# Performance work log

Measured on AMD Instinct MI355X. Metric: run time of the kernel, lower is better.

## Reference

```python
import jax, jax.numpy as jnp
import numpy as np

TEMPERATURE = 8.0  # sqrt(d_head=64)
CLAMP = 15.0
EPS = 1e-6


def setup_inputs() -> dict:
    key = jax.random.key(0)
    kq, kk, kv, km = jax.random.split(key, 4)
    B, Lq, Lk, D = 16, 2048, 2048, 64
    q = jax.random.normal(kq, (B, Lq, D), dtype=jnp.float32)
    k = jax.random.normal(kk, (B, Lk, D), dtype=jnp.float32)
    v = jax.random.normal(kv, (B, Lk, D), dtype=jnp.float32)
    mask = jax.random.randint(km, (B, Lq, Lk), 0, 2).astype(jnp.float32)
    return {"q": q, "k": k, "v": v, "mask": mask}


def masked_softmax(x, m, axis=-1):
    # clamp -> multiply by mask -> stable exp -> multiply by mask -> normalize
    x = jnp.clip(x, -CLAMP, CLAMP)
    x = x * m
    e_x = jnp.exp(x - jnp.max(x, axis=axis, keepdims=True))
    e_x = e_x * m
    return e_x / (jnp.sum(e_x, axis=axis, keepdims=True) + EPS)


def reference(q, k, v, mask):
    # scores: [B, Lq, Lk]
    attn = jnp.einsum('bqd,bkd->bqk', q, k) / TEMPERATURE
    attn = masked_softmax(attn, mask, axis=2)
    # dropout is identity in eval mode (deterministic reference)
    output = jnp.einsum('bqk,bkd->bqd', attn, v)
    return (output, attn)
```

## Files before the change

### kernel.cpp

```cpp
#include <hip/hip_runtime.h>
#include <stdint.h>

#define NB 16
#define LQ 2048
#define LK 2048
#define DH 64
#define QT 16

typedef short bf16x8 __attribute__((ext_vector_type(8)));
typedef float f32x4 __attribute__((ext_vector_type(4)));

__device__ __forceinline__ unsigned short f2bf(float f) {
    union { float f; uint32_t u; } v; v.f = f;
    uint32_t u = v.u;
    u += 0x7FFFu + ((u >> 16) & 1u);
    return (unsigned short)(u >> 16);
}
__device__ __forceinline__ float bf2f(unsigned short h) {
    union { uint32_t u; float f; } v; v.u = ((uint32_t)h) << 16;
    return v.f;
}
__device__ __forceinline__ uint32_t pack2(float lo, float hi) {
    return (uint32_t)f2bf(lo) | ((uint32_t)f2bf(hi) << 16);
}

__global__ void convert_kernel(const float* __restrict__ q, const float* __restrict__ k,
                               const float* __restrict__ v,
                               unsigned short* __restrict__ qb,
                               unsigned short* __restrict__ kb,
                               unsigned short* __restrict__ vtb) {
    int bid = blockIdx.x;
    int tid = threadIdx.x;
    if (bid < 2048) {
        const float* src = (bid < 1024) ? q : k;
        unsigned short* dst = (bid < 1024) ? qb : kb;
        int64_t off = (int64_t)(bid & 1023) * 2048 + (int64_t)tid * 8;
        float4 a = *(const float4*)(src + off);
        float4 b4 = *(const float4*)(src + off + 4);
        uint4 o;
        o.x = pack2(a.x, a.y);
        o.y = pack2(a.z, a.w);
        o.z = pack2(b4.x, b4.y);
        o.w = pack2(b4.z, b4.w);
        *(uint4*)(dst + off) = o;
    } else {
        __shared__ unsigned short tile[64][72];
        int bid2 = bid - 2048;
        int bb = bid2 >> 5, kt = bid2 & 31;
        int k0 = kt * 64;
        int krow = tid >> 2, dc = (tid & 3) * 16;
        const float* vp = v + ((int64_t)(bb * LK) + k0 + krow) * DH + dc;
        float4 x0 = *(const float4*)(vp);
        float4 x1 = *(const float4*)(vp + 4);
        float4 x2 = *(const float4*)(vp + 8);
        float4 x3 = *(const float4*)(vp + 12);
        float vals[16] = {x0.x, x0.y, x0.z, x0.w, x1.x, x1.y, x1.z, x1.w,
                          x2.x, x2.y, x2.z, x2.w, x3.x, x3.y, x3.z, x3.w};
        #pragma unroll
        for (int i = 0; i < 16; ++i) tile[dc + i][krow] = f2bf(vals[i]);
        __syncthreads();
        int d = tid >> 2, kc = (tid & 3) * 16;
        uint4 r0 = *(const uint4*)&tile[d][kc];
        uint4 r1 = *(const uint4*)&tile[d][kc + 8];
        unsigned short* op = vtb + ((int64_t)(bb * DH) + d) * LK + k0 + kc;
        *(uint4*)op = r0;
        *(uint4*)(op + 8) = r1;
    }
}

__launch_bounds__(512, 4)
__global__ void attn_kernel(const unsigned short* __restrict__ qb,
                            const unsigned short* __restrict__ kb,
                            const unsigned short* __restrict__ vtb,
                            const float* __restrict__ mask,
                            float* __restrict__ out, float* __restrict__ attn) {
    extern __shared__ char smem[];
    float* denom_part = (float*)(smem + QT * LK * 2);
    float* pp         = (float*)(smem + QT * LK * 2 + 512);

    int bid = blockIdx.x;
    int swz = (bid & 7) * 256 + (bid >> 3);
    int b = swz >> 7;
    int q0 = (swz & 127) * QT;

    int tid = threadIdx.x;
    int lane = tid & 63;
    int wave = tid >> 6;
    int lr = lane & 15, lg = lane >> 4;

    bf16x8 qf0, qf1;
    {
        const unsigned short* qp = qb + ((int64_t)(b * LQ + q0 + lr)) * DH + 8 * lg;
        qf0 = *(const bf16x8*)qp;
        qf1 = *(const bf16x8*)(qp + 32);
    }

    float dsum[4] = {0.f, 0.f, 0.f, 0.f};

    {
        const int64_t krow0 = (int64_t)b * LK;
        const float* mbase = mask + ((int64_t)(b * LQ + q0 + lg * 4)) * LK;
        bf16x8 kf0, kf1;
        float mr0, mr1, mr2, mr3;
        {
            const unsigned short* kp =
                kb + (krow0 + wave * 16 + lr) * DH + 8 * lg;
            kf0 = *(const bf16x8*)kp;
            kf1 = *(const bf16x8*)(kp + 32);
            const float* mp = mbase + wave * 16 + lr;
            mr0 = mp[0]; mr1 = mp[LK]; mr2 = mp[2 * LK]; mr3 = mp[3 * LK];
        }
        for (int kt = 0; kt < LK / 128; ++kt) {
            bf16x8 nk0, nk1;
            float nm0, nm1, nm2, nm3;
            if (kt < LK / 128 - 1) {
                int nbase = (kt + 1) * 128 + wave * 16;
                const unsigned short* kp = kb + (krow0 + nbase + lr) * DH + 8 * lg;
                nk0 = *(const bf16x8*)kp;
                nk1 = *(const bf16x8*)(kp + 32);
                const float* mp = mbase + nbase + lr;
                nm0 = mp[0]; nm1 = mp[LK]; nm2 = mp[2 * LK]; nm3 = mp[3 * LK];
            }
            f32x4 acc = {0.f, 0.f, 0.f, 0.f};
            acc = __builtin_amdgcn_mfma_f32_16x16x32_bf16(qf0, kf0, acc, 0, 0, 0);
            acc = __builtin_amdgcn_mfma_f32_16x16x32_bf16(qf1, kf1, acc, 0, 0, 0);
            int c = kt * 128 + wave * 16 + lr;
            float mv[4] = {mr0, mr1, mr2, mr3};
            #pragma unroll
            for (int j = 0; j < 4; ++j) {
                int r = lg * 4 + j;
                float s = acc[j] * 0.125f;
                s = fminf(fmaxf(s, -15.0f), 15.0f);
                float m = mv[j];
                float e = __expf(s * m) * m;
                unsigned short eb = f2bf(e);
                dsum[j] += bf2f(eb);
                int byteoff = (r * 4096 + c * 2) ^ ((r & 7) << 4);
                *(unsigned short*)(smem + byteoff) = eb;
            }
            kf0 = nk0; kf1 = nk1;
            mr0 = nm0; mr1 = nm1; mr2 = nm2; mr3 = nm3;
        }
    }

    #pragma unroll
    for (int j = 0; j < 4; ++j) {
        float s = dsum[j];
        s += __shfl_xor(s, 1);
        s += __shfl_xor(s, 2);
        s += __shfl_xor(s, 4);
        s += __shfl_xor(s, 8);
        if (lr == 0) denom_part[wave * 16 + lg * 4 + j] = s;
    }
    __syncthreads();

    f32x4 pacc = {0.f, 0.f, 0.f, 0.f};
    int cw = (wave & 3) * 16, kh = wave >> 2;
    {
        const unsigned short* vp =
            vtb + ((int64_t)(b * DH + cw + lr)) * LK + kh * 1024 + 8 * lg;
        int rowoff = lr * 4096;
        int sw = (lr & 7) << 4;
        int kk0 = kh * 1024;
        for (int kk = 0; kk < 1024; kk += 32) {
            int byteoff = (rowoff + (kk0 + kk + 8 * lg) * 2) ^ sw;
            bf16x8 ef = *(const bf16x8*)(smem + byteoff);
            bf16x8 vf = *(const bf16x8*)(vp + kk);
            pacc = __builtin_amdgcn_mfma_f32_16x16x32_bf16(ef, vf, pacc, 0, 0, 0);
        }
    }
    if (kh == 1) {
        #pragma unroll
        for (int j = 0; j < 4; ++j)
            pp[(wave & 3) * 256 + (lg * 4 + j) * 16 + lr] = pacc[j];
    }
    __syncthreads();
    if (kh == 0) {
        #pragma unroll
        for (int j = 0; j < 4; ++j) {
            int r = lg * 4 + j;
            float den = 1e-6f;
            #pragma unroll
            for (int w = 0; w < 8; ++w) den += denom_part[w * 16 + r];
            float val = pacc[j] + pp[cw * 16 + r * 16 + lr];
            out[((int64_t)(b * LQ + q0 + r)) * DH + cw + lr] = val / den;
        }
    }

    {
        int r = tid >> 5;
        float den = 1e-6f;
        #pragma unroll
        for (int w = 0; w < 8; ++w) den += denom_part[w * 16 + r];
        float inv = 1.0f / den;
        float* ap = attn + ((int64_t)(b * LQ + q0 + r)) * LK;
        int rowoff = r * 4096;
        int sw = (r & 7) << 4;
        for (int c0 = (tid & 31) * 8; c0 < LK; c0 += 256) {
            int byteoff = (rowoff + c0 * 2) ^ sw;
            bf16x8 ev = *(const bf16x8*)(smem + byteoff);
            float4 o0, o1;
            o0.x = bf2f((unsigned short)ev[0]) * inv;
            o0.y = bf2f((unsigned short)ev[1]) * inv;
            o0.z = bf2f((unsigned short)ev[2]) * inv;
            o0.w = bf2f((unsigned short)ev[3]) * inv;
            o1.x = bf2f((unsigned short)ev[4]) * inv;
            o1.y = bf2f((unsigned short)ev[5]) * inv;
            o1.z = bf2f((unsigned short)ev[6]) * inv;
            o1.w = bf2f((unsigned short)ev[7]) * inv;
            *(float4*)(ap + c0) = o0;
            *(float4*)(ap + c0 + 4) = o1;
        }
    }
}

extern "C" void kernel_launch(void* const* d_in, const int* in_sizes, int n_in,
                              void* d_out, int out_size, void* d_ws, size_t ws_size,
                              hipStream_t stream) {
    const float* q    = (const float*)d_in[0];
    const float* k    = (const float*)d_in[1];
    const float* v    = (const float*)d_in[2];
    const float* mask = (const float*)d_in[3];
    float* out  = (float*)d_out;
    float* attn = out + (int64_t)NB * LQ * DH;

    unsigned short* qb  = (unsigned short*)d_ws;
    unsigned short* kb  = qb + (int64_t)NB * LQ * DH;
    unsigned short* vtb = kb + (int64_t)NB * LK * DH;

    (void)hipFuncSetAttribute((const void*)attn_kernel,
                              hipFuncAttributeMaxDynamicSharedMemorySize, 70144);

    convert_kernel<<<2560, 256, 0, stream>>>(q, k, v, qb, kb, vtb);
    attn_kernel<<<2048, 512, 70144, stream>>>(qb, kb, vtb, mask, out, attn);
}
```

Before: 236.3 us.

## Use 16 waves per block, transpose QK MFMA for vectorized mask loads

Doubles the block to 1024 threads (16 waves), so each wave covers fewer key strips and the PV reduction is split four ways across waves, with partial sums combined through shared memory. The QK MFMA operands are swapped so each lane holds four consecutive key columns of one query row. That allows float4 mask loads and 8-byte packed bf16 stores to LDS instead of strided scalar mask loads and 2-byte stores. The aim is more memory-level parallelism on the mask and attn streams. In exchange it needs more shared memory per block and tighter register limits per thread.

```diff
diff --git a/kernel.cpp b/kernel.cpp
--- a/kernel.cpp
+++ b/kernel.cpp
@@ -6,6 +6,9 @@
 #define LK 2048
 #define DH 64
 #define QT 16
+#define NW 16
+#define STRIP (NW * 16)
+#define NIT (LK / STRIP)
 
 typedef short bf16x8 __attribute__((ext_vector_type(8)));
 typedef float f32x4 __attribute__((ext_vector_type(4)));
@@ -68,7 +71,7 @@
     }
 }
 
-__launch_bounds__(512, 4)
+__launch_bounds__(1024, 8)
 __global__ void attn_kernel(const unsigned short* __restrict__ qb,
                             const unsigned short* __restrict__ kb,
                             const unsigned short* __restrict__ vtb,
@@ -76,7 +79,7 @@
                             float* __restrict__ out, float* __restrict__ attn) {
     extern __shared__ char smem[];
     float* denom_part = (float*)(smem + QT * LK * 2);
-    float* pp         = (float*)(smem + QT * LK * 2 + 512);
+    float* pp         = (float*)(smem + QT * LK * 2 + 1024);
 
     int bid = blockIdx.x;
     int swz = (bid & 7) * 256 + (bid >> 3);
@@ -95,109 +98,100 @@
         qf1 = *(const bf16x8*)(qp + 32);
     }
 
-    float dsum[4] = {0.f, 0.f, 0.f, 0.f};
-
-    {
-        const int64_t krow0 = (int64_t)b * LK;
-        const float* mbase = mask + ((int64_t)(b * LQ + q0 + lg * 4)) * LK;
-        bf16x8 kf0, kf1;
-        float mr0, mr1, mr2, mr3;
-        {
-            const unsigned short* kp =
-                kb + (krow0 + wave * 16 + lr) * DH + 8 * lg;
-            kf0 = *(const bf16x8*)kp;
-            kf1 = *(const bf16x8*)(kp + 32);
-            const float* mp = mbase + wave * 16 + lr;
-            mr0 = mp[0]; mr1 = mp[LK]; mr2 = mp[2 * LK]; mr3 = mp[3 * LK];
-        }
-        for (int kt = 0; kt < LK / 128; ++kt) {
-            bf16x8 nk0, nk1;
-            float nm0, nm1, nm2, nm3;
-            if (kt < LK / 128 - 1) {
-                int nbase = (kt + 1) * 128 + wave * 16;
-                const unsigned short* kp = kb + (krow0 + nbase + lr) * DH + 8 * lg;
-                nk0 = *(const bf16x8*)kp;
-                nk1 = *(const bf16x8*)(kp + 32);
-                const float* mp = mbase + nbase + lr;
-                nm0 = mp[0]; nm1 = mp[LK]; nm2 = mp[2 * LK]; nm3 = mp[3 * LK];
-            }
+    float dsum = 0.f;
+
+    {
+        const unsigned short* kpw =
+            kb + (int64_t)b * LK * DH + (wave * 16 + lr) * DH + 8 * lg;
+        const float* mrow =
+            mask + ((int64_t)(b * LQ + q0 + lr)) * LK + wave * 16 + lg * 4;
+        float4 mf = *(const float4*)mrow;
+        #pragma unroll
+        for (int kt = 0; kt < NIT; ++kt) {
+            float4 nm;
+            if (kt < NIT - 1) nm = *(const float4*)(mrow + (kt + 1) * STRIP);
+            bf16x8 kf0 = *(const bf16x8*)(kpw + (int64_t)kt * STRIP * DH);
+            bf16x8 kf1 = *(const bf16x8*)(kpw + (int64_t)kt * STRIP * DH + 32);
             f32x4 acc = {0.f, 0.f, 0.f, 0.f};
-            acc = __builtin_amdgcn_mfma_f32_16x16x32_bf16(qf0, kf0, acc, 0, 0, 0);
-            acc = __builtin_amdgcn_mfma_f32_16x16x32_bf16(qf1, kf1, acc, 0, 0, 0);
-            int c = kt * 128 + wave * 16 + lr;
-            float mv[4] = {mr0, mr1, mr2, mr3};
+            acc = __builtin_amdgcn_mfma_f32_16x16x32_bf16(kf0, qf0, acc, 0, 0, 0);
+            acc = __builtin_amdgcn_mfma_f32_16x16x32_bf16(kf1, qf1, acc, 0, 0, 0);
+            float mv[4] = {mf.x, mf.y, mf.z, mf.w};
+            unsigned short eb[4];
             #pragma unroll
             for (int j = 0; j < 4; ++j) {
-                int r = lg * 4 + j;
                 float s = acc[j] * 0.125f;
                 s = fminf(fmaxf(s, -15.0f), 15.0f);
-                float m = mv[j];
-                float e = __expf(s * m) * m;
-                unsigned short eb = f2bf(e);
-                dsum[j] += bf2f(eb);
-                int byteoff = (r * 4096 + c * 2) ^ ((r & 7) << 4);
-                *(unsigned short*)(smem + byteoff) = eb;
+                float e = __expf(s * mv[j]) * mv[j];
+                eb[j] = f2bf(e);
+                dsum += bf2f(eb[j]);
             }
-            kf0 = nk0; kf1 = nk1;
-            mr0 = nm0; mr1 = nm1; mr2 = nm2; mr3 = nm3;
-        }
-    }
-
-    #pragma unroll
-    for (int j = 0; j < 4; ++j) {
-        float s = dsum[j];
-        s += __shfl_xor(s, 1);
-        s += __shfl_xor(s, 2);
-        s += __shfl_xor(s, 4);
-        s += __shfl_xor(s, 8);
-        if (lr == 0) denom_part[wave * 16 + lg * 4 + j] = s;
+            uint2 u;
+            u.x = (uint32_t)eb[0] | ((uint32_t)eb[1] << 16);
+            u.y = (uint32_t)eb[2] | ((uint32_t)eb[3] << 16);
+            int c = kt * STRIP + wave * 16 + lg * 4;
+            int byteoff = (lr * 4096 + c * 2) ^ ((lr & 7) << 4);
+            *(uint2*)(smem + byteoff) = u;
+            mf = nm;
+        }
+    }
+
+    {
+        float s = dsum;
+        s += __shfl_xor(s, 16);
+        s += __shfl_xor(s, 32);
+        if (lg == 0) denom_part[wave * 16 + lr] = s;
     }
     __syncthreads();
 
     f32x4 pacc = {0.f, 0.f, 0.f, 0.f};
-    int cw = (wave & 3) * 16, kh = wave >> 2;
+    int cw = (wave & 3) * 16, kq = wave >> 2;
     {
         const unsigned short* vp =
-            vtb + ((int64_t)(b * DH + cw + lr)) * LK + kh * 1024 + 8 * lg;
-        int rowoff = lr * 4096;
+            vtb + ((int64_t)(b * DH + cw + lr)) * LK + kq * 512 + 8 * lg;
+        int rowbase = lr * 4096;
         int sw = (lr & 7) << 4;
-        int kk0 = kh * 1024;
-        for (int kk = 0; kk < 1024; kk += 32) {
-            int byteoff = (rowoff + (kk0 + kk + 8 * lg) * 2) ^ sw;
+        int kk0 = kq * 512;
+        #pragma unroll 4
+        for (int kk = 0; kk < 512; kk += 32) {
+            int byteoff = (rowbase + (kk0 + kk + 8 * lg) * 2) ^ sw;
             bf16x8 ef = *(const bf16x8*)(smem + byteoff);
             bf16x8 vf = *(const bf16x8*)(vp + kk);
             pacc = __builtin_amdgcn_mfma_f32_16x16x32_bf16(ef, vf, pacc, 0, 0, 0);
         }
     }
-    if (kh == 1) {
+    if (kq != 0) {
         #pragma unroll
         for (int j = 0; j < 4; ++j)
-            pp[(wave & 3) * 256 + (lg * 4 + j) * 16 + lr] = pacc[j];
+            pp[((kq - 1) * 4 + (wave & 3)) * 256 + (lg * 4 + j) * 16 + lr] = pacc[j];
     }
     __syncthreads();
-    if (kh == 0) {
+    if (kq == 0) {
+        int c4 = wave & 3;
         #pragma unroll
         for (int j = 0; j < 4; ++j) {
             int r = lg * 4 + j;
             float den = 1e-6f;
             #pragma unroll
-            for (int w = 0; w < 8; ++w) den += denom_part[w * 16 + r];
-            float val = pacc[j] + pp[cw * 16 + r * 16 + lr];
+            for (int w = 0; w < NW; ++w) den += denom_part[w * 16 + r];
+            float val = pacc[j] + pp[(c4)*256 + r * 16 + lr] +
+                        pp[(4 + c4) * 256 + r * 16 + lr] +
+                        pp[(8 + c4) * 256 + r * 16 + lr];
             out[((int64_t)(b * LQ + q0 + r)) * DH + cw + lr] = val / den;
         }
     }
 
     {
-        int r = tid >> 5;
+        int r = tid >> 6;
         float den = 1e-6f;
         #pragma unroll
-        for (int w = 0; w < 8; ++w) den += denom_part[w * 16 + r];
+        for (int w = 0; w < NW; ++w) den += denom_part[w * 16 + r];
         float inv = 1.0f / den;
         float* ap = attn + ((int64_t)(b * LQ + q0 + r)) * LK;
-        int rowoff = r * 4096;
+        int rowbase = r * 4096;
         int sw = (r & 7) << 4;
-        for (int c0 = (tid & 31) * 8; c0 < LK; c0 += 256) {
-            int byteoff = (rowoff + c0 * 2) ^ sw;
+        #pragma unroll
+        for (int c0 = (tid & 63) * 8; c0 < LK; c0 += 512) {
+            int byteoff = (rowbase + c0 * 2) ^ sw;
             bf16x8 ev = *(const bf16x8*)(smem + byteoff);
             float4 o0, o1;
             o0.x = bf2f((unsigned short)ev[0]) * inv;
@@ -229,8 +223,8 @@
     unsigned short* vtb = kb + (int64_t)NB * LK * DH;
 
     (void)hipFuncSetAttribute((const void*)attn_kernel,
-                              hipFuncAttributeMaxDynamicSharedMemorySize, 70144);
+                              hipFuncAttributeMaxDynamicSharedMemorySize, 78848);
 
     convert_kernel<<<2560, 256, 0, stream>>>(q, k, v, qb, kb, vtb);
-    attn_kernel<<<2048, 512, 70144, stream>>>(qb, kb, vtb, mask, out, attn);
-}
+    attn_kernel<<<2048, 1024, 78848, stream>>>(qb, kb, vtb, mask, out, attn);
+}
```

New measurement: 230.8 us. -2.3%, faster.
